# Optimization experiments

Hardware: AMD Instinct MI355X
Metric: run time of the kernel (lower is better)

The kernel has to match this reference:

```python
import jax, jax.numpy as jnp
import numpy as np

N = 100000      # nodes
E = 800000      # directed edges (self-loops added in reference, PyG default)
F_IN = 16
H1, C1 = 3, 32  # conv1: heads=3, out=32 (concat -> 96)
H2, C2 = 1, 32  # conv2: heads=1, out=32
NC = 16         # n_channel
SLOPE = 0.2     # PyG GATConv default negative_slope


def setup_inputs() -> dict:
    key = jax.random.key(0)
    ks = jax.random.split(key, 12)
    s = 0.1
    return {
        "x": jax.random.normal(ks[0], (N, F_IN), jnp.float32),
        "edge_index": jax.random.randint(ks[1], (2, E), 0, N, dtype=jnp.int32),
        "W1": jax.random.normal(ks[2], (F_IN, H1 * C1), jnp.float32) * s,
        "a_src1": jax.random.normal(ks[3], (H1, C1), jnp.float32) * s,
        "a_dst1": jax.random.normal(ks[4], (H1, C1), jnp.float32) * s,
        "b1": jnp.zeros((H1 * C1,), jnp.float32),
        "W2": jax.random.normal(ks[5], (H1 * C1, H2 * C2), jnp.float32) * s,
        "a_src2": jax.random.normal(ks[6], (H2, C2), jnp.float32) * s,
        "a_dst2": jax.random.normal(ks[7], (H2, C2), jnp.float32) * s,
        "b2": jnp.zeros((H2 * C2,), jnp.float32),
        "Wf": jax.random.normal(ks[8], (C2, NC), jnp.float32) * s,
        "bf": jnp.zeros((NC,), jnp.float32),
    }


def _gat_layer(x, src, dst, W, a_s, a_d, b, heads, outc):
    # x: [N, Fin]; src/dst: [Etot]
    h = (x @ W).reshape(N, heads, outc)                        # [N, H, C]
    alpha_s = (h * a_s).sum(-1)                                # [N, H]
    alpha_d = (h * a_d).sum(-1)                                # [N, H]
    e = jax.nn.leaky_relu(alpha_s[src] + alpha_d[dst], SLOPE)  # [Etot, H]
    # scatter-softmax over edges grouped by destination node
    m = jax.ops.segment_max(e, dst, num_segments=N)            # [N, H]
    p = jnp.exp(e - m[dst])
    z = jax.ops.segment_sum(p, dst, num_segments=N)
    alpha = p / (z[dst] + 1e-16)                               # [Etot, H]
    out = jax.ops.segment_sum(h[src] * alpha[:, :, None], dst, num_segments=N)
    return out.reshape(N, heads * outc) + b


def reference(x, edge_index, W1, a_src1, a_dst1, b1, W2, a_src2, a_dst2, b2, Wf, bf):
    loops = jnp.arange(N, dtype=edge_index.dtype)  # PyG add_self_loops=True
    src = jnp.concatenate([edge_index[0], loops])
    dst = jnp.concatenate([edge_index[1], loops])
    h = jax.nn.selu(_gat_layer(x, src, dst, W1, a_src1, a_dst1, b1, H1, C1))
    h = jax.nn.selu(_gat_layer(h, src, dst, W2, a_src2, a_dst2, b2, H2, C2))
    return h @ Wf + bf
```

## Files before the change

### kernel.cpp

```cpp
#include <hip/hip_runtime.h>
#include <hip/hip_bf16.h>

#define N_NODES 100000
#define N_EDGES 800000
#define F_IN    16
#define H1      3
#define C1      32
#define F1      (H1*C1)
#define F2      32
#define NC      16
#define SLOPE       0.2f
#define SELU_SCALE  1.0507009873554805f
#define SELU_ALPHA  1.6732632423543772f

#define DEG_PAD 48

#define NSLICE        8
#define BLK_PER_SLICE 256
#define SCAT_BLKS     (NSLICE * BLK_PER_SLICE)
#define EDGES_PER_BLK (N_EDGES / BLK_PER_SLICE)
#define SLICE_NODES   (N_NODES / NSLICE)
#define XB_NB   ((N_NODES + 255) / 256)
#define BIN_CAP 512

typedef unsigned short ushort_t;

__device__ __forceinline__ ushort_t f2bf(float f) {
    unsigned u = __float_as_uint(f);
    return (ushort_t)((u + 0x7FFFu + ((u >> 16) & 1u)) >> 16);
}
__device__ __forceinline__ unsigned pack2bf(float a, float b) {
    return (unsigned)f2bf(a) | ((unsigned)f2bf(b) << 16);
}
__device__ __forceinline__ float bf_lo(unsigned u) { return __uint_as_float(u << 16); }
__device__ __forceinline__ float bf_hi(unsigned u) { return __uint_as_float(u & 0xFFFF0000u); }

__device__ __forceinline__ void unpack8(const uint4 v, float* f) {
    f[0] = bf_lo(v.x); f[1] = bf_hi(v.x);
    f[2] = bf_lo(v.y); f[3] = bf_hi(v.y);
    f[4] = bf_lo(v.z); f[5] = bf_hi(v.z);
    f[6] = bf_lo(v.w); f[7] = bf_hi(v.w);
}
__device__ __forceinline__ float selu_f(float u) {
    return u > 0.f ? SELU_SCALE * u : SELU_SCALE * SELU_ALPHA * (__expf(u) - 1.f);
}

__global__ __launch_bounds__(256) void bin_k(
    const int* __restrict__ ei, const float* __restrict__ x,
    const float* __restrict__ W1, const float* __restrict__ aS1,
    const float* __restrict__ aD1,
    uint2* __restrict__ binbuf, int* __restrict__ gcnt,
    uint4* __restrict__ xb, float4* __restrict__ as4, float4* __restrict__ ad4)
{
    __shared__ float swv[F_IN * 6];
    __shared__ int scnt;
    const int b = blockIdx.x, t = threadIdx.x;
    if (b < SCAT_BLKS) {
        if (t == 0) scnt = 0;
        __syncthreads();
        const int slice = b & 7;
        const int lo = slice * SLICE_NODES, hi = lo + SLICE_NODES;
        const int e0 = (b >> 3) * EDGES_PER_BLK;
        uint2* buf = binbuf + (size_t)b * BIN_CAP;
        const int lane = t & 63;
        for (int e = e0 + t; e < e0 + EDGES_PER_BLK; e += 256) {
            const int d = ei[N_EDGES + e];
            const bool pred = (d >= lo) && (d < hi);
            const unsigned long long mask = __ballot(pred);
            if (mask) {
                const int leader = (int)(__ffsll((unsigned long long)mask) - 1);
                int base = 0;
                if (lane == leader) base = atomicAdd(&scnt, (int)__popcll(mask));
                base = __shfl(base, leader);
                if (pred) {
                    const int off = (int)__popcll(mask & ((1ull << lane) - 1ull));
                    const int pos = min(base + off, BIN_CAP - 1);
                    buf[pos] = make_uint2((unsigned)ei[e], (unsigned)(d - lo));
                }
            }
        }
        __syncthreads();
        if (t == 0) gcnt[b] = min(scnt, BIN_CAP);
    } else {
        if (t < 96) {
            const int k = t / 6, j = t % 6;
            const int h = (j < 3) ? j : j - 3;
            const float* a = (j < 3) ? aS1 : aD1;
            float acc = 0.f;
#pragma unroll
            for (int c = 0; c < 32; ++c) acc += W1[k * F1 + h * 32 + c] * a[h * 32 + c];
            swv[k * 6 + j] = acc;
        }
        __syncthreads();
        const int node = (b - SCAT_BLKS) * 256 + t;
        if (node < N_NODES) {
            float xr[16];
            const float4* xp = reinterpret_cast<const float4*>(&x[(size_t)node * F_IN]);
            const float4 v0 = xp[0], v1 = xp[1], v2 = xp[2], v3 = xp[3];
            xr[0] = v0.x; xr[1] = v0.y; xr[2]  = v0.z; xr[3]  = v0.w;
            xr[4] = v1.x; xr[5] = v1.y; xr[6]  = v1.z; xr[7]  = v1.w;
            xr[8] = v2.x; xr[9] = v2.y; xr[10] = v2.z; xr[11] = v2.w;
            xr[12] = v3.x; xr[13] = v3.y; xr[14] = v3.z; xr[15] = v3.w;
            uint4 o0, o1;
            o0.x = pack2bf(xr[0], xr[1]);   o0.y = pack2bf(xr[2], xr[3]);
            o0.z = pack2bf(xr[4], xr[5]);   o0.w = pack2bf(xr[6], xr[7]);
            o1.x = pack2bf(xr[8], xr[9]);   o1.y = pack2bf(xr[10], xr[11]);
            o1.z = pack2bf(xr[12], xr[13]); o1.w = pack2bf(xr[14], xr[15]);
            xb[(size_t)node * 2]     = o0;
            xb[(size_t)node * 2 + 1] = o1;
            float sacc[3] = {0.f, 0.f, 0.f}, dacc[3] = {0.f, 0.f, 0.f};
#pragma unroll
            for (int k = 0; k < 16; ++k) {
                const float xk = xr[k];
#pragma unroll
                for (int j = 0; j < 3; ++j) {
                    sacc[j] += xk * swv[k * 6 + j];
                    dacc[j] += xk * swv[k * 6 + 3 + j];
                }
            }
            as4[node] = make_float4(sacc[0], sacc[1], sacc[2], 0.f);
            ad4[node] = make_float4(dacc[0], dacc[1], dacc[2], 0.f);
        }
    }
}

__global__ __launch_bounds__(256) void scat_k(
    const uint2* __restrict__ binbuf, const int* __restrict__ gcnt,
    int* __restrict__ deg, int* __restrict__ colp)
{
    const int b = blockIdx.x;
    const int slice = b & 7;
    const int lo = slice * SLICE_NODES;
    const int n = gcnt[b];
    const uint2* buf = binbuf + (size_t)b * BIN_CAP;
    int* cslice = colp + (size_t)slice * DEG_PAD * SLICE_NODES;
    for (int i = threadIdx.x; i < n; i += 256) {
        const uint2 e = buf[i];
        const int dl = (int)e.y;
        const int pos = atomicAdd(&deg[lo + dl], 1);
        if (pos < DEG_PAD) cslice[pos * SLICE_NODES + dl] = (int)e.x;
    }
}

__global__ __launch_bounds__(256) void agg1_k(
    const int* __restrict__ deg, const int* __restrict__ colp,
    const uint4* __restrict__ xb,
    const float4* __restrict__ as4, const float4* __restrict__ ad4,
    uint4* __restrict__ xagg_b)
{
    const int t = threadIdx.x;
    const int node = blockIdx.x * 64 + (t >> 2);
    const int u = t & 1;
    const int v = (t >> 1) & 1;
    if (node >= N_NODES) return;
    const int slice = node / SLICE_NODES;
    const int dl = node - slice * SLICE_NODES;
    const int* cbase = colp + (size_t)slice * DEG_PAD * SLICE_NODES + dl;
    const int dg = min(deg[node], DEG_PAD);
    const float4 adv = ad4[node];

    float acc[3][8];
#pragma unroll
    for (int h = 0; h < 3; ++h)
#pragma unroll
        for (int i = 0; i < 8; ++i) acc[h][i] = 0.f;
    float z0 = 0.f, z1 = 0.f, z2 = 0.f;
    if (v == 0) {
        const float4 a = as4[node];
        float e0 = a.x + adv.x; e0 = e0 > 0.f ? e0 : SLOPE * e0;
        float e1 = a.y + adv.y; e1 = e1 > 0.f ? e1 : SLOPE * e1;
        float e2 = a.z + adv.z; e2 = e2 > 0.f ? e2 : SLOPE * e2;
        const float p0 = __expf(e0), p1 = __expf(e1), p2 = __expf(e2);
        z0 = p0; z1 = p1; z2 = p2;
        float xf[8]; unpack8(xb[(size_t)node * 2 + u], xf);
#pragma unroll
        for (int i = 0; i < 8; ++i) {
            acc[0][i] = p0 * xf[i]; acc[1][i] = p1 * xf[i]; acc[2][i] = p2 * xf[i];
        }
    }
    int j = v; uint4 hv; float4 av;
    if (j < dg) { const int s = cbase[j * SLICE_NODES]; av = as4[s]; hv = xb[(size_t)s * 2 + u]; }
    while (j < dg) {
        const uint4 cx = hv; const float4 ca = av;
        const int jn = j + 2;
        if (jn < dg) {
            const int s = cbase[jn * SLICE_NODES];
            av = as4[s]; hv = xb[(size_t)s * 2 + u];
        }
        float e0 = ca.x + adv.x; e0 = e0 > 0.f ? e0 : SLOPE * e0;
        float e1 = ca.y + adv.y; e1 = e1 > 0.f ? e1 : SLOPE * e1;
        float e2 = ca.z + adv.z; e2 = e2 > 0.f ? e2 : SLOPE * e2;
        const float p0 = __expf(e0), p1 = __expf(e1), p2 = __expf(e2);
        z0 += p0; z1 += p1; z2 += p2;
        float xf[8]; unpack8(cx, xf);
#pragma unroll
        for (int i = 0; i < 8; ++i) {
            acc[0][i] += p0 * xf[i]; acc[1][i] += p1 * xf[i]; acc[2][i] += p2 * xf[i];
        }
        j = jn;
    }
    z0 += __shfl_xor(z0, 2); z1 += __shfl_xor(z1, 2); z2 += __shfl_xor(z2, 2);
#pragma unroll
    for (int h = 0; h < 3; ++h)
#pragma unroll
        for (int i = 0; i < 8; ++i) acc[h][i] += __shfl_xor(acc[h][i], 2);
    if (v == 0) {
        const float zi[3] = {1.f / (z0 + 1e-16f), 1.f / (z1 + 1e-16f), 1.f / (z2 + 1e-16f)};
#pragma unroll
        for (int h = 0; h < 3; ++h) {
            uint4 o;
            o.x = pack2bf(acc[h][0] * zi[h], acc[h][1] * zi[h]);
            o.y = pack2bf(acc[h][2] * zi[h], acc[h][3] * zi[h]);
            o.z = pack2bf(acc[h][4] * zi[h], acc[h][5] * zi[h]);
            o.w = pack2bf(acc[h][6] * zi[h], acc[h][7] * zi[h]);
            xagg_b[(size_t)node * 6 + h * 2 + u] = o;
        }
    }
}

__global__ __launch_bounds__(384) void l12_k(
    const uint4* __restrict__ xagg_b, const float* __restrict__ W1,
    const float* __restrict__ b1, const float* __restrict__ W2,
    const float* __restrict__ aS2, const float* __restrict__ aD2,
    ushort_t* __restrict__ h2b, float* __restrict__ as2, float* __restrict__ ad2)
{
    __shared__ float sxa[64 * 48];
    __shared__ float sx2[64][F1 + 1];
    __shared__ float swv[F1 * 2];
    const int t = threadIdx.x;
    const int node0 = blockIdx.x * 64;

    {
        const int nl = t / 6, w = t - nl * 6;
        const int node = node0 + nl;
        uint4 vv = make_uint4(0, 0, 0, 0);
        if (node < N_NODES) vv = xagg_b[(size_t)node * 6 + w];
        float xf[8]; unpack8(vv, xf);
        float* dst = &sxa[nl * 48 + w * 8];
        *reinterpret_cast<float4*>(dst)     = make_float4(xf[0], xf[1], xf[2], xf[3]);
        *reinterpret_cast<float4*>(dst + 4) = make_float4(xf[4], xf[5], xf[6], xf[7]);
    }
    if (t < 192) {
        const int k = t >> 1, j = t & 1;
        const float* a = j ? aD2 : aS2;
        float acc = 0.f;
#pragma unroll
        for (int c = 0; c < 32; ++c) acc += W2[k * F2 + c] * a[c];
        swv[k * 2 + j] = acc;
    }
    __syncthreads();

    {
        const int ng = t / 48;
        const int cp = t - ng * 48;
        const int c0 = cp * 2, c1 = c0 + 1;
        const int hc = c0 >> 5;
        float w0[16], w1[16];
#pragma unroll
        for (int k = 0; k < 16; ++k) { w0[k] = W1[k * F1 + c0]; w1[k] = W1[k * F1 + c1]; }
        const float bc0 = b1[c0], bc1 = b1[c1];
#pragma unroll
        for (int nn = 0; nn < 8; ++nn) {
            const int n = ng * 8 + nn;
            const float4* xp = reinterpret_cast<const float4*>(&sxa[n * 48 + hc * 16]);
            const float4 a0 = xp[0], a1 = xp[1], a2 = xp[2], a3 = xp[3];
            const float xa[16] = {a0.x, a0.y, a0.z, a0.w, a1.x, a1.y, a1.z, a1.w,
                                  a2.x, a2.y, a2.z, a2.w, a3.x, a3.y, a3.z, a3.w};
            float acc0 = bc0, acc1 = bc1;
#pragma unroll
            for (int k = 0; k < 16; ++k) { acc0 += xa[k] * w0[k]; acc1 += xa[k] * w1[k]; }
            sx2[n][c0] = selu_f(acc0);
            sx2[n][c1] = selu_f(acc1);
        }
    }
    __syncthreads();

    if (t < 256) {
        const int cq = t & 7;
        const int np = t >> 3;
        const int n0 = np * 2, n1 = n0 + 1;
        float acc0[4] = {0.f, 0.f, 0.f, 0.f}, acc1[4] = {0.f, 0.f, 0.f, 0.f};
#pragma unroll 4
        for (int k = 0; k < F1; ++k) {
            const float4 w = *reinterpret_cast<const float4*>(&W2[k * F2 + cq * 4]);
            const float x0 = sx2[n0][k], x1 = sx2[n1][k];
            acc0[0] += x0 * w.x; acc0[1] += x0 * w.y; acc0[2] += x0 * w.z; acc0[3] += x0 * w.w;
            acc1[0] += x1 * w.x; acc1[1] += x1 * w.y; acc1[2] += x1 * w.z; acc1[3] += x1 * w.w;
        }
        if (node0 + n0 < N_NODES) {
            uint2 o; o.x = pack2bf(acc0[0], acc0[1]); o.y = pack2bf(acc0[2], acc0[3]);
            *reinterpret_cast<uint2*>(&h2b[(size_t)(node0 + n0) * F2 + cq * 4]) = o;
        }
        if (node0 + n1 < N_NODES) {
            uint2 o; o.x = pack2bf(acc1[0], acc1[1]); o.y = pack2bf(acc1[2], acc1[3]);
            *reinterpret_cast<uint2*>(&h2b[(size_t)(node0 + n1) * F2 + cq * 4]) = o;
        }
        if (cq < 2) {
            float s0 = 0.f, s1 = 0.f;
#pragma unroll 4
            for (int k = 0; k < F1; ++k) {
                const float wv = swv[k * 2 + cq];
                s0 += sx2[n0][k] * wv; s1 += sx2[n1][k] * wv;
            }
            if (cq == 0) {
                if (node0 + n0 < N_NODES) as2[node0 + n0] = s0;
                if (node0 + n1 < N_NODES) as2[node0 + n1] = s1;
            } else {
                if (node0 + n0 < N_NODES) ad2[node0 + n0] = s0;
                if (node0 + n1 < N_NODES) ad2[node0 + n1] = s1;
            }
        }
    }
}

__global__ __launch_bounds__(256) void agg2_final_k(
    const int* __restrict__ deg, const int* __restrict__ colp,
    const ushort_t* __restrict__ hb,
    const float* __restrict__ as, const float* __restrict__ ad,
    const float* __restrict__ b2, const float* __restrict__ Wf,
    const float* __restrict__ bf, float* __restrict__ out)
{
    __shared__ float sW[F2 * NC];
    __shared__ float sx[64][33];
    const int t = threadIdx.x;
    for (int i = t; i < F2 * NC; i += 256) sW[i] = Wf[i];
    const int sub = t >> 2;
    const int u = t & 1;
    const int v = (t >> 1) & 1;
    const int node = blockIdx.x * 64 + sub;
    const bool valid = node < N_NODES;

    if (valid) {
        const int slice = node / SLICE_NODES;
        const int dl = node - slice * SLICE_NODES;
        const int* cbase = colp + (size_t)slice * DEG_PAD * SLICE_NODES + dl;
        const int dg = min(deg[node], DEG_PAD);
        const float adv = ad[node];
        float acc[16];
#pragma unroll
        for (int i = 0; i < 16; ++i) acc[i] = 0.f;
        float z = 0.f;
        if (v == 0) {
            float e = as[node] + adv; e = e > 0.f ? e : SLOPE * e;
            const float pv = __expf(e);
            z = pv;
            const uint4* hp = reinterpret_cast<const uint4*>(&hb[(size_t)node * F2 + u * 16]);
            float xf[8];
            unpack8(hp[0], xf);
#pragma unroll
            for (int i = 0; i < 8; ++i) acc[i] = pv * xf[i];
            unpack8(hp[1], xf);
#pragma unroll
            for (int i = 0; i < 8; ++i) acc[8 + i] = pv * xf[i];
        }
        int j = v; uint4 hva, hvb; float asv;
        if (j < dg) {
            const int s = cbase[j * SLICE_NODES];
            asv = as[s];
            const uint4* hp = reinterpret_cast<const uint4*>(&hb[(size_t)s * F2 + u * 16]);
            hva = hp[0]; hvb = hp[1];
        }
        while (j < dg) {
            const uint4 ca = hva, cb = hvb; const float cas = asv;
            const int jn = j + 2;
            if (jn < dg) {
                const int s = cbase[jn * SLICE_NODES];
                asv = as[s];
                const uint4* hp = reinterpret_cast<const uint4*>(&hb[(size_t)s * F2 + u * 16]);
                hva = hp[0]; hvb = hp[1];
            }
            float e = cas + adv; e = e > 0.f ? e : SLOPE * e;
            const float pv = __expf(e);
            z += pv;
            float xf[8];
            unpack8(ca, xf);
#pragma unroll
            for (int i = 0; i < 8; ++i) acc[i] += pv * xf[i];
            unpack8(cb, xf);
#pragma unroll
            for (int i = 0; i < 8; ++i) acc[8 + i] += pv * xf[i];
            j = jn;
        }
        z += __shfl_xor(z, 2);
#pragma unroll
        for (int i = 0; i < 16; ++i) acc[i] += __shfl_xor(acc[i], 2);
        if (v == 0) {
            const float zi = 1.f / (z + 1e-16f);
#pragma unroll
            for (int i = 0; i < 16; ++i)
                sx[sub][u * 16 + i] = selu_f(acc[i] * zi + b2[u * 16 + i]);
        }
    }
    __syncthreads();
    if (valid) {
        const int c0 = (t & 3) * 4;
        float r[4];
#pragma unroll
        for (int i = 0; i < 4; ++i) r[i] = bf[c0 + i];
#pragma unroll
        for (int k = 0; k < F2; ++k) {
            const float xk = sx[sub][k];
#pragma unroll
            for (int i = 0; i < 4; ++i) r[i] += xk * sW[k * NC + c0 + i];
        }
        *reinterpret_cast<float4*>(&out[(size_t)node * NC + c0]) =
            make_float4(r[0], r[1], r[2], r[3]);
    }
}

extern "C" void kernel_launch(void* const* d_in, const int* in_sizes, int n_in,
                              void* d_out, int out_size, void* d_ws, size_t ws_size,
                              hipStream_t stream)
{
    const float* x    = (const float*)d_in[0];
    const int*   ei   = (const int*)d_in[1];
    const float* W1   = (const float*)d_in[2];
    const float* aS1  = (const float*)d_in[3];
    const float* aD1  = (const float*)d_in[4];
    const float* b1   = (const float*)d_in[5];
    const float* W2   = (const float*)d_in[6];
    const float* aS2  = (const float*)d_in[7];
    const float* aD2  = (const float*)d_in[8];
    const float* b2   = (const float*)d_in[9];
    const float* Wf   = (const float*)d_in[10];
    const float* bf   = (const float*)d_in[11];
    float* out = (float*)d_out;

    uint4*    xb     = (uint4*)d_ws;
    float4*   as4    = (float4*)(xb + (size_t)N_NODES * 2);
    float4*   ad4    = as4 + N_NODES;
    uint4*    xagg_b = (uint4*)(ad4 + N_NODES);
    ushort_t* h2b    = (ushort_t*)(xagg_b + (size_t)N_NODES * 6);
    float*    as2    = (float*)(h2b + (size_t)N_NODES * F2);
    float*    ad2    = as2 + N_NODES;
    int*      colp   = (int*)(ad2 + N_NODES);
    int*      deg    = colp + (size_t)N_NODES * DEG_PAD;
    uint2*    binbuf = (uint2*)(deg + N_NODES);
    int*      gcnt   = (int*)(binbuf + (size_t)SCAT_BLKS * BIN_CAP);

    hipMemsetAsync(deg, 0, sizeof(int) * N_NODES, stream);
    bin_k<<<SCAT_BLKS + XB_NB, 256, 0, stream>>>(
        ei, x, W1, aS1, aD1, binbuf, gcnt, xb, as4, ad4);
    scat_k<<<SCAT_BLKS, 256, 0, stream>>>(binbuf, gcnt, deg, colp);
    agg1_k<<<(N_NODES + 63) / 64, 256, 0, stream>>>(deg, colp, xb, as4, ad4, xagg_b);
    l12_k<<<(N_NODES + 63) / 64, 384, 0, stream>>>(
        xagg_b, W1, b1, W2, aS2, aD2, h2b, as2, ad2);
    agg2_final_k<<<(N_NODES + 63) / 64, 256, 0, stream>>>(
        deg, colp, h2b, as2, ad2, b2, Wf, bf, out);
}
```

Measured before the change: 148.7 us.

## Fuse edge binning with CSR scatter and fuse layer-1 aggregation with linear layers

Edge binning now keeps each block's bin in shared memory and scatters straight into the padded column list, which removes the separate scatter kernel and the global bin buffer round trip. The layer-1 attention aggregation is merged into the following linear kernel, with aggregated features written to shared memory instead of a bf16 global buffer, so the xagg buffer and one launch go away. In exchange the fused kernel runs at 256 threads instead of 384, and the middle GEMV stage now loops twice per thread. Aggregated features also stay in fp32 rather than being rounded to bf16.

```diff
diff --git a/kernel.cpp b/kernel.cpp
--- a/kernel.cpp
+++ b/kernel.cpp
@@ -45,15 +45,16 @@
     return u > 0.f ? SELU_SCALE * u : SELU_SCALE * SELU_ALPHA * (__expf(u) - 1.f);
 }
 
-__global__ __launch_bounds__(256) void bin_k(
+__global__ __launch_bounds__(256) void build_k(
     const int* __restrict__ ei, const float* __restrict__ x,
     const float* __restrict__ W1, const float* __restrict__ aS1,
     const float* __restrict__ aD1,
-    uint2* __restrict__ binbuf, int* __restrict__ gcnt,
+    int* __restrict__ deg, int* __restrict__ colp,
     uint4* __restrict__ xb, float4* __restrict__ as4, float4* __restrict__ ad4)
 {
+    __shared__ uint2 sbuf[BIN_CAP];
+    __shared__ int scnt;
     __shared__ float swv[F_IN * 6];
-    __shared__ int scnt;
     const int b = blockIdx.x, t = threadIdx.x;
     if (b < SCAT_BLKS) {
         if (t == 0) scnt = 0;
@@ -61,7 +62,6 @@
         const int slice = b & 7;
         const int lo = slice * SLICE_NODES, hi = lo + SLICE_NODES;
         const int e0 = (b >> 3) * EDGES_PER_BLK;
-        uint2* buf = binbuf + (size_t)b * BIN_CAP;
         const int lane = t & 63;
         for (int e = e0 + t; e < e0 + EDGES_PER_BLK; e += 256) {
             const int d = ei[N_EDGES + e];
@@ -75,12 +75,19 @@
                 if (pred) {
                     const int off = (int)__popcll(mask & ((1ull << lane) - 1ull));
                     const int pos = min(base + off, BIN_CAP - 1);
-                    buf[pos] = make_uint2((unsigned)ei[e], (unsigned)(d - lo));
+                    sbuf[pos] = make_uint2((unsigned)ei[e], (unsigned)(d - lo));
                 }
             }
         }
         __syncthreads();
-        if (t == 0) gcnt[b] = min(scnt, BIN_CAP);
+        const int n = min(scnt, BIN_CAP);
+        int* cslice = colp + (size_t)slice * DEG_PAD * SLICE_NODES;
+        for (int i = t; i < n; i += 256) {
+            const uint2 e = sbuf[i];
+            const int dl = (int)e.y;
+            const int pos = atomicAdd(&deg[lo + dl], 1);
+            if (pos < DEG_PAD) cslice[pos * SLICE_NODES + dl] = (int)e.x;
+        }
     } else {
         if (t < 96) {
             const int k = t / 6, j = t % 6;
@@ -124,103 +131,12 @@
     }
 }
 
-__global__ __launch_bounds__(256) void scat_k(
-    const uint2* __restrict__ binbuf, const int* __restrict__ gcnt,
-    int* __restrict__ deg, int* __restrict__ colp)
-{
-    const int b = blockIdx.x;
-    const int slice = b & 7;
-    const int lo = slice * SLICE_NODES;
-    const int n = gcnt[b];
-    const uint2* buf = binbuf + (size_t)b * BIN_CAP;
-    int* cslice = colp + (size_t)slice * DEG_PAD * SLICE_NODES;
-    for (int i = threadIdx.x; i < n; i += 256) {
-        const uint2 e = buf[i];
-        const int dl = (int)e.y;
-        const int pos = atomicAdd(&deg[lo + dl], 1);
-        if (pos < DEG_PAD) cslice[pos * SLICE_NODES + dl] = (int)e.x;
-    }
-}
-
-__global__ __launch_bounds__(256) void agg1_k(
+__global__ __launch_bounds__(256) void agg1_l12_k(
     const int* __restrict__ deg, const int* __restrict__ colp,
     const uint4* __restrict__ xb,
     const float4* __restrict__ as4, const float4* __restrict__ ad4,
-    uint4* __restrict__ xagg_b)
-{
-    const int t = threadIdx.x;
-    const int node = blockIdx.x * 64 + (t >> 2);
-    const int u = t & 1;
-    const int v = (t >> 1) & 1;
-    if (node >= N_NODES) return;
-    const int slice = node / SLICE_NODES;
-    const int dl = node - slice * SLICE_NODES;
-    const int* cbase = colp + (size_t)slice * DEG_PAD * SLICE_NODES + dl;
-    const int dg = min(deg[node], DEG_PAD);
-    const float4 adv = ad4[node];
-
-    float acc[3][8];
-#pragma unroll
-    for (int h = 0; h < 3; ++h)
-#pragma unroll
-        for (int i = 0; i < 8; ++i) acc[h][i] = 0.f;
-    float z0 = 0.f, z1 = 0.f, z2 = 0.f;
-    if (v == 0) {
-        const float4 a = as4[node];
-        float e0 = a.x + adv.x; e0 = e0 > 0.f ? e0 : SLOPE * e0;
-        float e1 = a.y + adv.y; e1 = e1 > 0.f ? e1 : SLOPE * e1;
-        float e2 = a.z + adv.z; e2 = e2 > 0.f ? e2 : SLOPE * e2;
-        const float p0 = __expf(e0), p1 = __expf(e1), p2 = __expf(e2);
-        z0 = p0; z1 = p1; z2 = p2;
-        float xf[8]; unpack8(xb[(size_t)node * 2 + u], xf);
-#pragma unroll
-        for (int i = 0; i < 8; ++i) {
-            acc[0][i] = p0 * xf[i]; acc[1][i] = p1 * xf[i]; acc[2][i] = p2 * xf[i];
-        }
-    }
-    int j = v; uint4 hv; float4 av;
-    if (j < dg) { const int s = cbase[j * SLICE_NODES]; av = as4[s]; hv = xb[(size_t)s * 2 + u]; }
-    while (j < dg) {
-        const uint4 cx = hv; const float4 ca = av;
-        const int jn = j + 2;
-        if (jn < dg) {
-            const int s = cbase[jn * SLICE_NODES];
-            av = as4[s]; hv = xb[(size_t)s * 2 + u];
-        }
-        float e0 = ca.x + adv.x; e0 = e0 > 0.f ? e0 : SLOPE * e0;
-        float e1 = ca.y + adv.y; e1 = e1 > 0.f ? e1 : SLOPE * e1;
-        float e2 = ca.z + adv.z; e2 = e2 > 0.f ? e2 : SLOPE * e2;
-        const float p0 = __expf(e0), p1 = __expf(e1), p2 = __expf(e2);
-        z0 += p0; z1 += p1; z2 += p2;
-        float xf[8]; unpack8(cx, xf);
-#pragma unroll
-        for (int i = 0; i < 8; ++i) {
-            acc[0][i] += p0 * xf[i]; acc[1][i] += p1 * xf[i]; acc[2][i] += p2 * xf[i];
-        }
-        j = jn;
-    }
-    z0 += __shfl_xor(z0, 2); z1 += __shfl_xor(z1, 2); z2 += __shfl_xor(z2, 2);
-#pragma unroll
-    for (int h = 0; h < 3; ++h)
-#pragma unroll
-        for (int i = 0; i < 8; ++i) acc[h][i] += __shfl_xor(acc[h][i], 2);
-    if (v == 0) {
-        const float zi[3] = {1.f / (z0 + 1e-16f), 1.f / (z1 + 1e-16f), 1.f / (z2 + 1e-16f)};
-#pragma unroll
-        for (int h = 0; h < 3; ++h) {
-            uint4 o;
-            o.x = pack2bf(acc[h][0] * zi[h], acc[h][1] * zi[h]);
-            o.y = pack2bf(acc[h][2] * zi[h], acc[h][3] * zi[h]);
-            o.z = pack2bf(acc[h][4] * zi[h], acc[h][5] * zi[h]);
-            o.w = pack2bf(acc[h][6] * zi[h], acc[h][7] * zi[h]);
-            xagg_b[(size_t)node * 6 + h * 2 + u] = o;
-        }
-    }
-}
-
-__global__ __launch_bounds__(384) void l12_k(
-    const uint4* __restrict__ xagg_b, const float* __restrict__ W1,
-    const float* __restrict__ b1, const float* __restrict__ W2,
+    const float* __restrict__ W1, const float* __restrict__ b1,
+    const float* __restrict__ W2,
     const float* __restrict__ aS2, const float* __restrict__ aD2,
     ushort_t* __restrict__ h2b, float* __restrict__ as2, float* __restrict__ ad2)
 {
@@ -230,16 +146,6 @@
     const int t = threadIdx.x;
     const int node0 = blockIdx.x * 64;
 
-    {
-        const int nl = t / 6, w = t - nl * 6;
-        const int node = node0 + nl;
-        uint4 vv = make_uint4(0, 0, 0, 0);
-        if (node < N_NODES) vv = xagg_b[(size_t)node * 6 + w];
-        float xf[8]; unpack8(vv, xf);
-        float* dst = &sxa[nl * 48 + w * 8];
-        *reinterpret_cast<float4*>(dst)     = make_float4(xf[0], xf[1], xf[2], xf[3]);
-        *reinterpret_cast<float4*>(dst + 4) = make_float4(xf[4], xf[5], xf[6], xf[7]);
-    }
     if (t < 192) {
         const int k = t >> 1, j = t & 1;
         const float* a = j ? aD2 : aS2;
@@ -248,11 +154,91 @@
         for (int c = 0; c < 32; ++c) acc += W2[k * F2 + c] * a[c];
         swv[k * 2 + j] = acc;
     }
+
+    {
+        const int nl = t >> 2;
+        const int node = node0 + nl;
+        const int u = t & 1;
+        const int v = (t >> 1) & 1;
+        if (node < N_NODES) {
+            const int slice = node / SLICE_NODES;
+            const int dl = node - slice * SLICE_NODES;
+            const int* cbase = colp + (size_t)slice * DEG_PAD * SLICE_NODES + dl;
+            const int dg = min(deg[node], DEG_PAD);
+            const float4 adv = ad4[node];
+            float acc[3][8];
+#pragma unroll
+            for (int h = 0; h < 3; ++h)
+#pragma unroll
+                for (int i = 0; i < 8; ++i) acc[h][i] = 0.f;
+            float z0 = 0.f, z1 = 0.f, z2 = 0.f;
+            if (v == 0) {
+                const float4 a = as4[node];
+                float e0 = a.x + adv.x; e0 = e0 > 0.f ? e0 : SLOPE * e0;
+                float e1 = a.y + adv.y; e1 = e1 > 0.f ? e1 : SLOPE * e1;
+                float e2 = a.z + adv.z; e2 = e2 > 0.f ? e2 : SLOPE * e2;
+                const float p0 = __expf(e0), p1 = __expf(e1), p2 = __expf(e2);
+                z0 = p0; z1 = p1; z2 = p2;
+                float xf[8]; unpack8(xb[(size_t)node * 2 + u], xf);
+#pragma unroll
+                for (int i = 0; i < 8; ++i) {
+                    acc[0][i] = p0 * xf[i]; acc[1][i] = p1 * xf[i]; acc[2][i] = p2 * xf[i];
+                }
+            }
+            int j = v; uint4 hv; float4 av;
+            if (j < dg) { const int s = cbase[j * SLICE_NODES]; av = as4[s]; hv = xb[(size_t)s * 2 + u]; }
+            while (j < dg) {
+                const uint4 cx = hv; const float4 ca = av;
+                const int jn = j + 2;
+                if (jn < dg) {
+                    const int s = cbase[jn * SLICE_NODES];
+                    av = as4[s]; hv = xb[(size_t)s * 2 + u];
+                }
+                float e0 = ca.x + adv.x; e0 = e0 > 0.f ? e0 : SLOPE * e0;
+                float e1 = ca.y + adv.y; e1 = e1 > 0.f ? e1 : SLOPE * e1;
+                float e2 = ca.z + adv.z; e2 = e2 > 0.f ? e2 : SLOPE * e2;
+                const float p0 = __expf(e0), p1 = __expf(e1), p2 = __expf(e2);
+                z0 += p0; z1 += p1; z2 += p2;
+                float xf[8]; unpack8(cx, xf);
+#pragma unroll
+                for (int i = 0; i < 8; ++i) {
+                    acc[0][i] += p0 * xf[i]; acc[1][i] += p1 * xf[i]; acc[2][i] += p2 * xf[i];
+                }
+                j = jn;
+            }
+            z0 += __shfl_xor(z0, 2); z1 += __shfl_xor(z1, 2); z2 += __shfl_xor(z2, 2);
+#pragma unroll
+            for (int h = 0; h < 3; ++h)
+#pragma unroll
+                for (int i = 0; i < 8; ++i) acc[h][i] += __shfl_xor(acc[h][i], 2);
+            if (v == 0) {
+                const float zi[3] = {1.f / (z0 + 1e-16f), 1.f / (z1 + 1e-16f),
+                                     1.f / (z2 + 1e-16f)};
+#pragma unroll
+                for (int h = 0; h < 3; ++h) {
+                    float* dst = &sxa[nl * 48 + h * 16 + u * 8];
+                    *reinterpret_cast<float4*>(dst) =
+                        make_float4(acc[h][0] * zi[h], acc[h][1] * zi[h],
+                                    acc[h][2] * zi[h], acc[h][3] * zi[h]);
+                    *reinterpret_cast<float4*>(dst + 4) =
+                        make_float4(acc[h][4] * zi[h], acc[h][5] * zi[h],
+                                    acc[h][6] * zi[h], acc[h][7] * zi[h]);
+                }
+            }
+        } else if (v == 0) {
+#pragma unroll
+            for (int h = 0; h < 3; ++h) {
+                float* dst = &sxa[nl * 48 + h * 16 + u * 8];
+                *reinterpret_cast<float4*>(dst)     = make_float4(0.f, 0.f, 0.f, 0.f);
+                *reinterpret_cast<float4*>(dst + 4) = make_float4(0.f, 0.f, 0.f, 0.f);
+            }
+        }
+    }
     __syncthreads();
 
-    {
-        const int ng = t / 48;
-        const int cp = t - ng * 48;
+    for (int tt = t; tt < 384; tt += 256) {
+        const int ng = tt / 48;
+        const int cp = tt - ng * 48;
         const int c0 = cp * 2, c1 = c0 + 1;
         const int hc = c0 >> 5;
         float w0[16], w1[16];
@@ -275,7 +261,7 @@
     }
     __syncthreads();
 
-    if (t < 256) {
+    {
         const int cq = t & 7;
         const int np = t >> 3;
         const int n0 = np * 2, n1 = n0 + 1;
@@ -426,25 +412,20 @@
     const float* bf   = (const float*)d_in[11];
     float* out = (float*)d_out;
 
-    uint4*    xb     = (uint4*)d_ws;
-    float4*   as4    = (float4*)(xb + (size_t)N_NODES * 2);
-    float4*   ad4    = as4 + N_NODES;
-    uint4*    xagg_b = (uint4*)(ad4 + N_NODES);
-    ushort_t* h2b    = (ushort_t*)(xagg_b + (size_t)N_NODES * 6);
-    float*    as2    = (float*)(h2b + (size_t)N_NODES * F2);
-    float*    ad2    = as2 + N_NODES;
-    int*      colp   = (int*)(ad2 + N_NODES);
-    int*      deg    = colp + (size_t)N_NODES * DEG_PAD;
-    uint2*    binbuf = (uint2*)(deg + N_NODES);
-    int*      gcnt   = (int*)(binbuf + (size_t)SCAT_BLKS * BIN_CAP);
+    uint4*    xb   = (uint4*)d_ws;
+    float4*   as4  = (float4*)(xb + (size_t)N_NODES * 2);
+    float4*   ad4  = as4 + N_NODES;
+    ushort_t* h2b  = (ushort_t*)(ad4 + N_NODES);
+    float*    as2  = (float*)(h2b + (size_t)N_NODES * F2);
+    float*    ad2  = as2 + N_NODES;
+    int*      colp = (int*)(ad2 + N_NODES);
+    int*      deg  = colp + (size_t)N_NODES * DEG_PAD;
 
     hipMemsetAsync(deg, 0, sizeof(int) * N_NODES, stream);
-    bin_k<<<SCAT_BLKS + XB_NB, 256, 0, stream>>>(
-        ei, x, W1, aS1, aD1, binbuf, gcnt, xb, as4, ad4);
-    scat_k<<<SCAT_BLKS, 256, 0, stream>>>(binbuf, gcnt, deg, colp);
-    agg1_k<<<(N_NODES + 63) / 64, 256, 0, stream>>>(deg, colp, xb, as4, ad4, xagg_b);
-    l12_k<<<(N_NODES + 63) / 64, 384, 0, stream>>>(
-        xagg_b, W1, b1, W2, aS2, aD2, h2b, as2, ad2);
+    build_k<<<SCAT_BLKS + XB_NB, 256, 0, stream>>>(
+        ei, x, W1, aS1, aD1, deg, colp, xb, as4, ad4);
+    agg1_l12_k<<<(N_NODES + 63) / 64, 256, 0, stream>>>(
+        deg, colp, xb, as4, ad4, W1, b1, W2, aS2, aD2, h2b, as2, ad2);
     agg2_final_k<<<(N_NODES + 63) / 64, 256, 0, stream>>>(
         deg, colp, h2b, as2, ad2, b2, Wf, bf, out);
 }
```

Result: faster. 140.8 us (-5.3%).
